# Kernel optimization log

Measured on AMD Instinct MI355X. Metric: run time of the kernel, lower is better.

Reference implementation:

```python
import jax, jax.numpy as jnp
import numpy as np

N_NODES = 100000
N_EDGES = 1600000
N_GRAPHS = 256
F_NODE, F_EDGE, HID, OUT = 64, 16, 128, 128
BN_SCALE = 1.0 / np.sqrt(1.0 + 1e-5)  # BatchNorm eval with running mean 0, var 1


def setup_inputs() -> dict:
    key = jax.random.key(0)
    ks = iter(jax.random.split(key, 64))
    inp = {}
    inp["x"] = jax.random.normal(next(ks), (N_NODES, F_NODE), dtype=jnp.float32)
    inp["edge_attr"] = jax.random.normal(next(ks), (N_EDGES, F_EDGE), dtype=jnp.float32)
    inp["edge_index"] = jax.random.randint(next(ks), (2, N_EDGES), 0, N_NODES)
    inp["batch"] = jnp.sort(jax.random.randint(next(ks), (N_NODES,), 0, N_GRAPHS))

    def p(shape, scale):
        return (jax.random.normal(next(ks), shape, dtype=jnp.float32) * scale)

    in_dims = [F_NODE, HID, HID]
    for i, d in enumerate(in_dims):
        inp[f"el_w{i}"] = p((F_EDGE, d), F_EDGE ** -0.5)
        inp[f"el_b{i}"] = jnp.zeros((d,), jnp.float32)
        inp[f"c{i}_w1"] = p((d, HID), d ** -0.5)
        inp[f"c{i}_b1"] = jnp.zeros((HID,), jnp.float32)
        inp[f"c{i}_g"] = jnp.ones((HID,), jnp.float32)
        inp[f"c{i}_bt"] = jnp.zeros((HID,), jnp.float32)
        inp[f"c{i}_w2"] = p((HID, HID), HID ** -0.5)
        inp[f"c{i}_b2"] = jnp.zeros((HID,), jnp.float32)
    inp["o_w1"] = p((HID, OUT), HID ** -0.5)
    inp["o_b1"] = jnp.zeros((OUT,), jnp.float32)
    inp["o_w2"] = p((OUT, OUT), OUT ** -0.5)
    inp["o_b2"] = jnp.zeros((OUT,), jnp.float32)
    return inp


def reference(x, edge_attr,
              el_w0, el_b0, c0_w1, c0_b1, c0_g, c0_bt, c0_w2, c0_b2,
              el_w1, el_b1, c1_w1, c1_b1, c1_g, c1_bt, c1_w2, c1_b2,
              el_w2, el_b2, c2_w1, c2_b1, c2_g, c2_bt, c2_w2, c2_b2,
              o_w1, o_b1, o_w2, o_b2,
              edge_index, batch):
    src, dst = edge_index[0], edge_index[1]
    n = x.shape[0]
    layers = [
        (el_w0, el_b0, c0_w1, c0_b1, c0_g, c0_bt, c0_w2, c0_b2),
        (el_w1, el_b1, c1_w1, c1_b1, c1_g, c1_bt, c1_w2, c1_b2),
        (el_w2, el_b2, c2_w1, c2_b1, c2_g, c2_bt, c2_w2, c2_b2),
    ]
    h = x
    for (ew, eb, w1, b1, g, bt, w2, b2) in layers:
        ea = edge_attr @ ew + eb                              # [E, d]
        msg = jax.nn.relu(h[src] + ea)                        # GINEConv message
        agg = jax.ops.segment_sum(msg, dst, num_segments=n)   # scatter-sum to targets
        hh = h + agg                                          # (1+eps)*x + aggr, eps=0
        hh = hh @ w1 + b1                                     # MLP: Linear
        hh = g * (hh * BN_SCALE) + bt                         # BatchNorm1d (eval)
        hh = jax.nn.relu(hh)
        hh = hh @ w2 + b2                                     # MLP: Linear
        h = jax.nn.relu(hh)                                   # dropout(p=0, eval) + act
    s = jax.ops.segment_sum(h, batch, num_segments=N_GRAPHS)
    cnt = jax.ops.segment_sum(jnp.ones((n,), h.dtype), batch, num_segments=N_GRAPHS)
    pooled = s / jnp.maximum(cnt, 1.0)[:, None]               # scatter-mean pooling
    out = jax.nn.relu(pooled @ o_w1 + o_b1) @ o_w2 + o_b2     # out_lin
    return out
```

## Files before the change

kernel.cpp:

```cpp
#include <hip/hip_runtime.h>
#include <hip/hip_fp16.h>
#include <cstdint>
#include <cstddef>

#define N_NODES_C  100000
#define N_EDGES_C  1600000
#define N_GRAPHS_C 256
#define HID_C      128
#define BN_SCALE_C 0.9999950000374997f

#define SCAN_B 1024
#define SCAN_NB ((N_NODES_C + SCAN_B - 1) / SCAN_B)

typedef _Float16 h2 __attribute__((ext_vector_type(2)));
typedef _Float16 h4 __attribute__((ext_vector_type(4)));
typedef _Float16 h8 __attribute__((ext_vector_type(8)));
typedef float    f4 __attribute__((ext_vector_type(4)));

struct __align__(16) EA8 { h2 p[4]; };
struct __align__(8)  HQ  { h2 a, b; };
struct __align__(16) H8 { __half2 v[4]; };

#if defined(__has_builtin)
#  if __has_builtin(__builtin_amdgcn_fdot2)
#    define HAVE_FDOT2 1
#  endif
#endif
#ifndef HAVE_FDOT2
#  define HAVE_FDOT2 0
#endif

__device__ __forceinline__ float fdot2_(h2 a, h2 b, float c)
{
#if HAVE_FDOT2
    return __builtin_amdgcn_fdot2(a, b, c, false);
#else
    return c + (float)a[0] * (float)b[0] + (float)a[1] * (float)b[1];
#endif
}

__global__ __launch_bounds__(256) void hist_kernel(
    const int* __restrict__ dst, int* __restrict__ counts, int n_edges)
{
    int e = blockIdx.x * 256 + threadIdx.x;
    if (e < n_edges) atomicAdd(&counts[dst[e]], 1);
}

__global__ __launch_bounds__(SCAN_B) void scan1_kernel(
    const int* __restrict__ counts, int* __restrict__ incl,
    int* __restrict__ blocksums, int n)
{
    __shared__ int sdata[SCAN_B];
    const int lid = threadIdx.x;
    const int i = blockIdx.x * SCAN_B + lid;
    sdata[lid] = (i < n) ? counts[i] : 0;
    __syncthreads();
#pragma unroll
    for (int off = 1; off < SCAN_B; off <<= 1) {
        int t = (lid >= off) ? sdata[lid - off] : 0;
        __syncthreads();
        sdata[lid] += t;
        __syncthreads();
    }
    if (i < n) incl[i] = sdata[lid];
    if (lid == SCAN_B - 1) blocksums[blockIdx.x] = sdata[lid];
}

__global__ void scan2_kernel(const int* __restrict__ blocksums,
                             int* __restrict__ blockoffs, int nb)
{
    if (threadIdx.x == 0 && blockIdx.x == 0) {
        int off = 0;
        for (int b = 0; b < nb; ++b) { blockoffs[b] = off; off += blocksums[b]; }
    }
}

__global__ __launch_bounds__(SCAN_B) void scan3_kernel(
    int* __restrict__ incl, const int* __restrict__ blockoffs, int n)
{
    const int i = blockIdx.x * SCAN_B + threadIdx.x;
    if (i < n) incl[i] += blockoffs[blockIdx.x];
}

__global__ __launch_bounds__(256) void initrows_kernel(
    const int* __restrict__ incl, const int* __restrict__ counts,
    int* __restrict__ rowstart, int* __restrict__ cursor, int n)
{
    const int i = blockIdx.x * 256 + threadIdx.x;
    if (i < n) {
        const int rs = incl[i] - counts[i];
        rowstart[i] = rs;
        cursor[i]   = rs;
    }
}

__global__ __launch_bounds__(256) void scatter_kernel(
    const int* __restrict__ src, const int* __restrict__ dst,
    int* __restrict__ cursor, int* __restrict__ perm_src,
    int* __restrict__ perm_eid, int n_edges)
{
    const int e = blockIdx.x * 256 + threadIdx.x;
    if (e < n_edges) {
        const int pos = atomicAdd(&cursor[dst[e]], 1);
        perm_src[pos] = src[e];
        perm_eid[pos] = e;
    }
}

__global__ __launch_bounds__(256) void permute_ea_f16_kernel(
    const float* __restrict__ edge_attr, const int* __restrict__ perm_eid,
    __half* __restrict__ ea_f16, int n_edges)
{
    const int j = blockIdx.x * 256 + threadIdx.x;
    if (j >= n_edges) return;
    const int eid = perm_eid[j];
    const float4* p = (const float4*)(edge_attr + (size_t)eid * 16);
    const float4 q0 = p[0], q1 = p[1], q2 = p[2], q3 = p[3];
    H8 a, b;
    a.v[0] = __floats2half2_rn(q0.x, q0.y);
    a.v[1] = __floats2half2_rn(q0.z, q0.w);
    a.v[2] = __floats2half2_rn(q1.x, q1.y);
    a.v[3] = __floats2half2_rn(q1.z, q1.w);
    b.v[0] = __floats2half2_rn(q2.x, q2.y);
    b.v[1] = __floats2half2_rn(q2.z, q2.w);
    b.v[2] = __floats2half2_rn(q3.x, q3.y);
    b.v[3] = __floats2half2_rn(q3.z, q3.w);
    H8* o = (H8*)(ea_f16 + (size_t)j * 16);
    o[0] = a;
    o[1] = b;
}

__global__ __launch_bounds__(256) void cast_f16_kernel(
    const float* __restrict__ in, _Float16* __restrict__ out, int n4)
{
    const int i = blockIdx.x * 256 + threadIdx.x;
    if (i >= n4) return;
    const float4 v = ((const float4*)in)[i];
    h4 o; o[0] = (_Float16)v.x; o[1] = (_Float16)v.y;
    o[2] = (_Float16)v.z; o[3] = (_Float16)v.w;
    *(h4*)(out + (size_t)i * 4) = o;
}

__global__ __launch_bounds__(256) void transpose_w_kernel(
    const float* __restrict__ w, _Float16* __restrict__ wt, int K, int N)
{
    const int i = blockIdx.x * 256 + threadIdx.x;
    if (i >= K * N) return;
    const int n = i / K;
    const int k = i - n * K;
    wt[(size_t)n * K + k] = (_Float16)w[(size_t)k * N + n];
}

template<int DIN, bool LASTL>
__global__ __launch_bounds__(128) void gine_layer_kernel(
    const _Float16* __restrict__ hin,
    const _Float16* __restrict__ ea16,
    const int* __restrict__ perm_src,
    const int* __restrict__ rowstart, const int* __restrict__ rowend,
    const float* __restrict__ ew, const float* __restrict__ eb,
    const _Float16* __restrict__ w1t, const float* __restrict__ b1,
    const float* __restrict__ gm, const float* __restrict__ bt,
    const _Float16* __restrict__ w2t, const float* __restrict__ b2,
    float* __restrict__ hout, _Float16* __restrict__ h16out, int n_tiles)
{
    constexpr int SXP = DIN + 8;
    constexpr int STP = HID_C + 8;
    __shared__ _Float16 s_x[2][16][SXP];
    __shared__ _Float16 s_t[2][16][STP];

    const int w    = threadIdx.x >> 6;
    const int lane = threadIdx.x & 63;
    int tile = blockIdx.x * 2 + w;
    if (tile >= n_tiles) tile = n_tiles - 1;
    const int node0 = tile * 16;

    constexpr int NQ  = DIN / 4;
    constexpr int GPW = 64 / NQ;
    constexpr int NPG = 16 / GPW;
    const int fq = lane & (NQ - 1);
    const int g  = lane / NQ;

    h2 ew2h[8][4];
#pragma unroll
    for (int k2 = 0; k2 < 8; ++k2)
#pragma unroll
        for (int fi = 0; fi < 4; ++fi) {
            h2 t;
            t[0] = (_Float16)ew[(size_t)(2 * k2)     * DIN + fq * 4 + fi];
            t[1] = (_Float16)ew[(size_t)(2 * k2 + 1) * DIN + fq * 4 + fi];
            ew2h[k2][fi] = t;
        }
    const float4 ebv = *(const float4*)(eb + fq * 4);

#pragma unroll
    for (int i = 0; i < NPG; ++i) {
        const int ni = g * NPG + i;
        const int v  = node0 + ni;
        const int s0 = rowstart[v];
        const int s1 = rowend[v];

        float4 acc = {0.f, 0.f, 0.f, 0.f};
        int j = s0;
        for (; j + 2 <= s1; j += 2) {
            const int sn0 = perm_src[j + 0];
            const int sn1 = perm_src[j + 1];
            const HQ hq0 = *(const HQ*)(hin + (size_t)sn0 * DIN + fq * 4);
            const HQ hq1 = *(const HQ*)(hin + (size_t)sn1 * DIN + fq * 4);
            const EA8* pe = (const EA8*)(ea16 + (size_t)j * 16);
            const EA8 a0 = pe[0], c0 = pe[1], a1 = pe[2], c1 = pe[3];
            float4 m0 = {ebv.x, ebv.y, ebv.z, ebv.w};
            float4 m1 = m0;
#pragma unroll
            for (int k = 0; k < 4; ++k) {
                m0.x = fdot2_(a0.p[k], ew2h[k][0], m0.x);
                m0.y = fdot2_(a0.p[k], ew2h[k][1], m0.y);
                m0.z = fdot2_(a0.p[k], ew2h[k][2], m0.z);
                m0.w = fdot2_(a0.p[k], ew2h[k][3], m0.w);
                m1.x = fdot2_(a1.p[k], ew2h[k][0], m1.x);
                m1.y = fdot2_(a1.p[k], ew2h[k][1], m1.y);
                m1.z = fdot2_(a1.p[k], ew2h[k][2], m1.z);
                m1.w = fdot2_(a1.p[k], ew2h[k][3], m1.w);
            }
#pragma unroll
            for (int k = 0; k < 4; ++k) {
                m0.x = fdot2_(c0.p[k], ew2h[4 + k][0], m0.x);
                m0.y = fdot2_(c0.p[k], ew2h[4 + k][1], m0.y);
                m0.z = fdot2_(c0.p[k], ew2h[4 + k][2], m0.z);
                m0.w = fdot2_(c0.p[k], ew2h[4 + k][3], m0.w);
                m1.x = fdot2_(c1.p[k], ew2h[4 + k][0], m1.x);
                m1.y = fdot2_(c1.p[k], ew2h[4 + k][1], m1.y);
                m1.z = fdot2_(c1.p[k], ew2h[4 + k][2], m1.z);
                m1.w = fdot2_(c1.p[k], ew2h[4 + k][3], m1.w);
            }
            acc.x += fmaxf(m0.x + (float)hq0.a[0], 0.f) + fmaxf(m1.x + (float)hq1.a[0], 0.f);
            acc.y += fmaxf(m0.y + (float)hq0.a[1], 0.f) + fmaxf(m1.y + (float)hq1.a[1], 0.f);
            acc.z += fmaxf(m0.z + (float)hq0.b[0], 0.f) + fmaxf(m1.z + (float)hq1.b[0], 0.f);
            acc.w += fmaxf(m0.w + (float)hq0.b[1], 0.f) + fmaxf(m1.w + (float)hq1.b[1], 0.f);
        }
        if (j < s1) {
            const int sn = perm_src[j];
            const HQ hq = *(const HQ*)(hin + (size_t)sn * DIN + fq * 4);
            const EA8* pe = (const EA8*)(ea16 + (size_t)j * 16);
            const EA8 a0 = pe[0], c0 = pe[1];
            float4 m0 = {ebv.x, ebv.y, ebv.z, ebv.w};
#pragma unroll
            for (int k = 0; k < 4; ++k) {
                m0.x = fdot2_(a0.p[k], ew2h[k][0], m0.x);
                m0.y = fdot2_(a0.p[k], ew2h[k][1], m0.y);
                m0.z = fdot2_(a0.p[k], ew2h[k][2], m0.z);
                m0.w = fdot2_(a0.p[k], ew2h[k][3], m0.w);
            }
#pragma unroll
            for (int k = 0; k < 4; ++k) {
                m0.x = fdot2_(c0.p[k], ew2h[4 + k][0], m0.x);
                m0.y = fdot2_(c0.p[k], ew2h[4 + k][1], m0.y);
                m0.z = fdot2_(c0.p[k], ew2h[4 + k][2], m0.z);
                m0.w = fdot2_(c0.p[k], ew2h[4 + k][3], m0.w);
            }
            acc.x += fmaxf(m0.x + (float)hq.a[0], 0.f);
            acc.y += fmaxf(m0.y + (float)hq.a[1], 0.f);
            acc.z += fmaxf(m0.z + (float)hq.b[0], 0.f);
            acc.w += fmaxf(m0.w + (float)hq.b[1], 0.f);
        }

        const HQ hv = *(const HQ*)(hin + (size_t)v * DIN + fq * 4);
        h4 o;
        o[0] = (_Float16)(acc.x + (float)hv.a[0]);
        o[1] = (_Float16)(acc.y + (float)hv.a[1]);
        o[2] = (_Float16)(acc.z + (float)hv.b[0]);
        o[3] = (_Float16)(acc.w + (float)hv.b[1]);
        *(h4*)&s_x[w][ni][fq * 4] = o;
    }
    __syncthreads();

    const int ln   = lane & 15;
    const int quad = lane >> 4;

#pragma unroll
    for (int nt = 0; nt < 8; ++nt) {
        const int col = nt * 16 + ln;
        const float bv = b1[col];
        f4 acc = {bv, bv, bv, bv};
#pragma unroll
        for (int ks = 0; ks < DIN / 32; ++ks) {
            const h8 af = *(const h8*)&s_x[w][ln][ks * 32 + quad * 8];
            const h8 bf = *(const h8*)(w1t + (size_t)col * DIN + ks * 32 + quad * 8);
            acc = __builtin_amdgcn_mfma_f32_16x16x32_f16(af, bf, acc, 0, 0, 0);
        }
        const float gv = gm[col], btv = bt[col];
#pragma unroll
        for (int r = 0; r < 4; ++r) {
            const float t = fmaxf(fmaf(acc[r] * BN_SCALE_C, gv, btv), 0.f);
            s_t[w][quad * 4 + r][col] = (_Float16)t;
        }
    }
    __syncthreads();

#pragma unroll
    for (int nt = 0; nt < 8; ++nt) {
        const int col = nt * 16 + ln;
        const float bv = b2[col];
        f4 acc = {bv, bv, bv, bv};
#pragma unroll
        for (int ks = 0; ks < HID_C / 32; ++ks) {
            const h8 af = *(const h8*)&s_t[w][ln][ks * 32 + quad * 8];
            const h8 bf = *(const h8*)(w2t + (size_t)col * HID_C + ks * 32 + quad * 8);
            acc = __builtin_amdgcn_mfma_f32_16x16x32_f16(af, bf, acc, 0, 0, 0);
        }
#pragma unroll
        for (int r = 0; r < 4; ++r) {
            const int node = node0 + quad * 4 + r;
            const float v = fmaxf(acc[r], 0.f);
            if (LASTL) {
                hout[(size_t)node * HID_C + col] = v;
            } else {
                h16out[(size_t)node * HID_C + col] = (_Float16)v;
            }
        }
    }
}

__global__ __launch_bounds__(256) void pool_kernel(
    const float* __restrict__ hfin, const int* __restrict__ batch,
    const float* __restrict__ w1, const float* __restrict__ b1,
    const float* __restrict__ w2, const float* __restrict__ b2,
    float* __restrict__ out, int n_nodes)
{
    const int gid = blockIdx.x;

    int lo = 0, hi = n_nodes;
    while (lo < hi) { int mid = (lo + hi) >> 1; if (batch[mid] < gid) lo = mid + 1; else hi = mid; }
    const int start = lo;
    hi = n_nodes;
    while (lo < hi) { int mid = (lo + hi) >> 1; if (batch[mid] < gid + 1) lo = mid + 1; else hi = mid; }
    const int end = lo;

    const int f = threadIdx.x & (HID_C - 1);
    const int half = threadIdx.x >> 7;

    float sum = 0.f;
    for (int n = start + half; n < end; n += 2)
        sum += hfin[(size_t)n * HID_C + f];

    __shared__ float s_sum[2][HID_C];
    __shared__ float s_p[HID_C];
    __shared__ float s_t[HID_C];
    s_sum[half][f] = sum;
    __syncthreads();

    if (threadIdx.x < HID_C) {
        const float cnt = (float)(end - start);
        s_p[f] = (s_sum[0][f] + s_sum[1][f]) / fmaxf(cnt, 1.f);
    }
    __syncthreads();

    if (threadIdx.x < HID_C) {
        float acc = b1[f];
        for (int k = 0; k < HID_C; ++k) acc = fmaf(s_p[k], w1[k * HID_C + f], acc);
        s_t[f] = fmaxf(acc, 0.f);
    }
    __syncthreads();

    if (threadIdx.x < HID_C) {
        float acc = b2[f];
        for (int k = 0; k < HID_C; ++k) acc = fmaf(s_t[k], w2[k * HID_C + f], acc);
        out[(size_t)gid * HID_C + f] = acc;
    }
}

extern "C" void kernel_launch(void* const* d_in, const int* in_sizes, int n_in,
                              void* d_out, int out_size, void* d_ws, size_t ws_size,
                              hipStream_t stream)
{
    const float* x         = (const float*)d_in[0];
    const float* edge_attr = (const float*)d_in[1];
    const int*   edge_index= (const int*)  d_in[2];
    const int*   batch     = (const int*)  d_in[3];
    const int*   src = edge_index;
    const int*   dst = edge_index + N_EDGES_C;

    const float* el_w[3] = {(const float*)d_in[4],  (const float*)d_in[12], (const float*)d_in[20]};
    const float* el_b[3] = {(const float*)d_in[5],  (const float*)d_in[13], (const float*)d_in[21]};
    const float* c_w1[3] = {(const float*)d_in[6],  (const float*)d_in[14], (const float*)d_in[22]};
    const float* c_b1[3] = {(const float*)d_in[7],  (const float*)d_in[15], (const float*)d_in[23]};
    const float* c_g [3] = {(const float*)d_in[8],  (const float*)d_in[16], (const float*)d_in[24]};
    const float* c_bt[3] = {(const float*)d_in[9],  (const float*)d_in[17], (const float*)d_in[25]};
    const float* c_w2[3] = {(const float*)d_in[10], (const float*)d_in[18], (const float*)d_in[26]};
    const float* c_b2[3] = {(const float*)d_in[11], (const float*)d_in[19], (const float*)d_in[27]};
    const float* o_w1 = (const float*)d_in[28];
    const float* o_b1 = (const float*)d_in[29];
    const float* o_w2 = (const float*)d_in[30];
    const float* o_b2 = (const float*)d_in[31];

    char* wsp = (char*)d_ws;
    size_t used = 0;
    auto alloc = [&](size_t bytes) { char* p = wsp + used; used += (bytes + 255) & ~(size_t)255; return p; };
    float* h        = (float*)alloc((size_t)N_NODES_C * HID_C * 4);
    int*   counts   = (int*)alloc((size_t)N_NODES_C * 4);
    int*   incl     = (int*)alloc((size_t)N_NODES_C * 4);
    int*   rowstart = (int*)alloc((size_t)N_NODES_C * 4);
    int*   cursor   = (int*)alloc((size_t)N_NODES_C * 4);
    int*   blocksums= (int*)alloc(128 * 4);
    int*   blockoffs= (int*)alloc(128 * 4);
    int*   perm_src = (int*)alloc((size_t)N_EDGES_C * 4);
    int*   perm_eid = (int*)alloc((size_t)N_EDGES_C * 4);
    _Float16* ea_f16 = (_Float16*)alloc((size_t)N_EDGES_C * 16 * 2);
    _Float16* h16_a  = (_Float16*)alloc((size_t)N_NODES_C * HID_C * 2);
    _Float16* h16_b  = (_Float16*)alloc((size_t)N_NODES_C * HID_C * 2);
    _Float16* x_f16  = (_Float16*)alloc((size_t)N_NODES_C * 64 * 2);
    _Float16* w1t[3], *w2t[3];
    for (int l = 0; l < 3; ++l) {
        w1t[l] = (_Float16*)alloc((size_t)HID_C * HID_C * 2);
        w2t[l] = (_Float16*)alloc((size_t)HID_C * HID_C * 2);
    }
    (void)ws_size;

    hipMemsetAsync(counts, 0, (size_t)N_NODES_C * 4, stream);
    hist_kernel<<<(N_EDGES_C + 255) / 256, 256, 0, stream>>>(dst, counts, N_EDGES_C);
    scan1_kernel<<<SCAN_NB, SCAN_B, 0, stream>>>(counts, incl, blocksums, N_NODES_C);
    scan2_kernel<<<1, 64, 0, stream>>>(blocksums, blockoffs, SCAN_NB);
    scan3_kernel<<<SCAN_NB, SCAN_B, 0, stream>>>(incl, blockoffs, N_NODES_C);
    initrows_kernel<<<(N_NODES_C + 255) / 256, 256, 0, stream>>>(incl, counts, rowstart,
                                                                 cursor, N_NODES_C);
    scatter_kernel<<<(N_EDGES_C + 255) / 256, 256, 0, stream>>>(src, dst, cursor,
                                                                perm_src, perm_eid, N_EDGES_C);
    permute_ea_f16_kernel<<<(N_EDGES_C + 255) / 256, 256, 0, stream>>>(
        edge_attr, perm_eid, (__half*)ea_f16, N_EDGES_C);
    cast_f16_kernel<<<(N_NODES_C * 64 / 4 + 255) / 256, 256, 0, stream>>>(
        x, x_f16, N_NODES_C * 64 / 4);
    for (int l = 0; l < 3; ++l) {
        const int K1 = (l == 0) ? 64 : HID_C;
        transpose_w_kernel<<<(K1 * HID_C + 255) / 256, 256, 0, stream>>>(
            c_w1[l], w1t[l], K1, HID_C);
        transpose_w_kernel<<<(HID_C * HID_C + 255) / 256, 256, 0, stream>>>(
            c_w2[l], w2t[l], HID_C, HID_C);
    }

    const int n_tiles = N_NODES_C / 16;
    const int nb = (n_tiles + 1) / 2;

    gine_layer_kernel<64, false><<<nb, 128, 0, stream>>>(
        x_f16, ea_f16, perm_src, rowstart, incl,
        el_w[0], el_b[0], w1t[0], c_b1[0], c_g[0], c_bt[0], w2t[0], c_b2[0],
        h, h16_a, n_tiles);
    gine_layer_kernel<128, false><<<nb, 128, 0, stream>>>(
        h16_a, ea_f16, perm_src, rowstart, incl,
        el_w[1], el_b[1], w1t[1], c_b1[1], c_g[1], c_bt[1], w2t[1], c_b2[1],
        h, h16_b, n_tiles);
    gine_layer_kernel<128, true><<<nb, 128, 0, stream>>>(
        h16_b, ea_f16, perm_src, rowstart, incl,
        el_w[2], el_b[2], w1t[2], c_b1[2], c_g[2], c_bt[2], w2t[2], c_b2[2],
        h, h16_a, n_tiles);

    pool_kernel<<<N_GRAPHS_C, 256, 0, stream>>>(h, batch, o_w1, o_b1, o_w2, o_b2,
                                                (float*)d_out, N_NODES_C);
}
```

Before: 1.048 ms.

## Split fused GINE layer into separate aggregation and MFMA MLP kernels

Each fused layer kernel is split in two. A gather/aggregation kernel assigns one node per thread group across 256-thread blocks and writes the aggregated fp16 features to a global buffer. A separate 64-thread MFMA kernel then runs the two-layer MLP per 16-node tile. The perm_src and perm_eid arrays are also merged into one interleaved int2 array. The aim is better load balance and occupancy in the irregular gather phase, with no node-tile imbalance stalling the MFMA stage, at the cost of an extra global round trip for the aggregated features and extra launches.

Measured after the change: 1.066 ms. No clear change (+1.8%).

```diff
diff --git a/kernel.cpp b/kernel.cpp
--- a/kernel.cpp
+++ b/kernel.cpp
@@ -19,7 +19,7 @@
 
 struct __align__(16) EA8 { h2 p[4]; };
 struct __align__(8)  HQ  { h2 a, b; };
-struct __align__(16) H8 { __half2 v[4]; };
+struct __align__(16) H8  { __half2 v[4]; };
 
 #if defined(__has_builtin)
 #  if __has_builtin(__builtin_amdgcn_fdot2)
@@ -96,24 +96,22 @@
 
 __global__ __launch_bounds__(256) void scatter_kernel(
     const int* __restrict__ src, const int* __restrict__ dst,
-    int* __restrict__ cursor, int* __restrict__ perm_src,
-    int* __restrict__ perm_eid, int n_edges)
+    int* __restrict__ cursor, int2* __restrict__ perm_se, int n_edges)
 {
     const int e = blockIdx.x * 256 + threadIdx.x;
     if (e < n_edges) {
         const int pos = atomicAdd(&cursor[dst[e]], 1);
-        perm_src[pos] = src[e];
-        perm_eid[pos] = e;
+        perm_se[pos] = make_int2(src[e], e);
     }
 }
 
 __global__ __launch_bounds__(256) void permute_ea_f16_kernel(
-    const float* __restrict__ edge_attr, const int* __restrict__ perm_eid,
+    const float* __restrict__ edge_attr, const int2* __restrict__ perm_se,
     __half* __restrict__ ea_f16, int n_edges)
 {
     const int j = blockIdx.x * 256 + threadIdx.x;
     if (j >= n_edges) return;
-    const int eid = perm_eid[j];
+    const int eid = perm_se[j].y;
     const float4* p = (const float4*)(edge_attr + (size_t)eid * 16);
     const float4 q0 = p[0], q1 = p[1], q2 = p[2], q3 = p[3];
     H8 a, b;
@@ -151,34 +149,20 @@
     wt[(size_t)n * K + k] = (_Float16)w[(size_t)k * N + n];
 }
 
-template<int DIN, bool LASTL>
-__global__ __launch_bounds__(128) void gine_layer_kernel(
-    const _Float16* __restrict__ hin,
-    const _Float16* __restrict__ ea16,
-    const int* __restrict__ perm_src,
+template<int DIN>
+__global__ __launch_bounds__(256) void gine_agg_kernel(
+    const _Float16* __restrict__ hin, const _Float16* __restrict__ ea16,
+    const int2* __restrict__ perm_se,
     const int* __restrict__ rowstart, const int* __restrict__ rowend,
     const float* __restrict__ ew, const float* __restrict__ eb,
-    const _Float16* __restrict__ w1t, const float* __restrict__ b1,
-    const float* __restrict__ gm, const float* __restrict__ bt,
-    const _Float16* __restrict__ w2t, const float* __restrict__ b2,
-    float* __restrict__ hout, _Float16* __restrict__ h16out, int n_tiles)
-{
-    constexpr int SXP = DIN + 8;
-    constexpr int STP = HID_C + 8;
-    __shared__ _Float16 s_x[2][16][SXP];
-    __shared__ _Float16 s_t[2][16][STP];
-
-    const int w    = threadIdx.x >> 6;
-    const int lane = threadIdx.x & 63;
-    int tile = blockIdx.x * 2 + w;
-    if (tile >= n_tiles) tile = n_tiles - 1;
-    const int node0 = tile * 16;
-
-    constexpr int NQ  = DIN / 4;
-    constexpr int GPW = 64 / NQ;
-    constexpr int NPG = 16 / GPW;
-    const int fq = lane & (NQ - 1);
-    const int g  = lane / NQ;
+    _Float16* __restrict__ x16, int n_nodes)
+{
+    constexpr int NQ    = DIN / 4;
+    constexpr int SLOTS = 256 / NQ;
+    const int fq   = threadIdx.x & (NQ - 1);
+    const int slot = threadIdx.x / NQ;
+    const int v = blockIdx.x * SLOTS + slot;
+    if (v >= n_nodes) return;
 
     h2 ew2h[8][4];
 #pragma unroll
@@ -192,89 +176,104 @@
         }
     const float4 ebv = *(const float4*)(eb + fq * 4);
 
-#pragma unroll
-    for (int i = 0; i < NPG; ++i) {
-        const int ni = g * NPG + i;
-        const int v  = node0 + ni;
-        const int s0 = rowstart[v];
-        const int s1 = rowend[v];
-
-        float4 acc = {0.f, 0.f, 0.f, 0.f};
-        int j = s0;
-        for (; j + 2 <= s1; j += 2) {
-            const int sn0 = perm_src[j + 0];
-            const int sn1 = perm_src[j + 1];
-            const HQ hq0 = *(const HQ*)(hin + (size_t)sn0 * DIN + fq * 4);
-            const HQ hq1 = *(const HQ*)(hin + (size_t)sn1 * DIN + fq * 4);
-            const EA8* pe = (const EA8*)(ea16 + (size_t)j * 16);
-            const EA8 a0 = pe[0], c0 = pe[1], a1 = pe[2], c1 = pe[3];
-            float4 m0 = {ebv.x, ebv.y, ebv.z, ebv.w};
-            float4 m1 = m0;
-#pragma unroll
-            for (int k = 0; k < 4; ++k) {
-                m0.x = fdot2_(a0.p[k], ew2h[k][0], m0.x);
-                m0.y = fdot2_(a0.p[k], ew2h[k][1], m0.y);
-                m0.z = fdot2_(a0.p[k], ew2h[k][2], m0.z);
-                m0.w = fdot2_(a0.p[k], ew2h[k][3], m0.w);
-                m1.x = fdot2_(a1.p[k], ew2h[k][0], m1.x);
-                m1.y = fdot2_(a1.p[k], ew2h[k][1], m1.y);
-                m1.z = fdot2_(a1.p[k], ew2h[k][2], m1.z);
-                m1.w = fdot2_(a1.p[k], ew2h[k][3], m1.w);
-            }
-#pragma unroll
-            for (int k = 0; k < 4; ++k) {
-                m0.x = fdot2_(c0.p[k], ew2h[4 + k][0], m0.x);
-                m0.y = fdot2_(c0.p[k], ew2h[4 + k][1], m0.y);
-                m0.z = fdot2_(c0.p[k], ew2h[4 + k][2], m0.z);
-                m0.w = fdot2_(c0.p[k], ew2h[4 + k][3], m0.w);
-                m1.x = fdot2_(c1.p[k], ew2h[4 + k][0], m1.x);
-                m1.y = fdot2_(c1.p[k], ew2h[4 + k][1], m1.y);
-                m1.z = fdot2_(c1.p[k], ew2h[4 + k][2], m1.z);
-                m1.w = fdot2_(c1.p[k], ew2h[4 + k][3], m1.w);
-            }
-            acc.x += fmaxf(m0.x + (float)hq0.a[0], 0.f) + fmaxf(m1.x + (float)hq1.a[0], 0.f);
-            acc.y += fmaxf(m0.y + (float)hq0.a[1], 0.f) + fmaxf(m1.y + (float)hq1.a[1], 0.f);
-            acc.z += fmaxf(m0.z + (float)hq0.b[0], 0.f) + fmaxf(m1.z + (float)hq1.b[0], 0.f);
-            acc.w += fmaxf(m0.w + (float)hq0.b[1], 0.f) + fmaxf(m1.w + (float)hq1.b[1], 0.f);
-        }
-        if (j < s1) {
-            const int sn = perm_src[j];
-            const HQ hq = *(const HQ*)(hin + (size_t)sn * DIN + fq * 4);
-            const EA8* pe = (const EA8*)(ea16 + (size_t)j * 16);
-            const EA8 a0 = pe[0], c0 = pe[1];
-            float4 m0 = {ebv.x, ebv.y, ebv.z, ebv.w};
-#pragma unroll
-            for (int k = 0; k < 4; ++k) {
-                m0.x = fdot2_(a0.p[k], ew2h[k][0], m0.x);
-                m0.y = fdot2_(a0.p[k], ew2h[k][1], m0.y);
-                m0.z = fdot2_(a0.p[k], ew2h[k][2], m0.z);
-                m0.w = fdot2_(a0.p[k], ew2h[k][3], m0.w);
-            }
-#pragma unroll
-            for (int k = 0; k < 4; ++k) {
-                m0.x = fdot2_(c0.p[k], ew2h[4 + k][0], m0.x);
-                m0.y = fdot2_(c0.p[k], ew2h[4 + k][1], m0.y);
-                m0.z = fdot2_(c0.p[k], ew2h[4 + k][2], m0.z);
-                m0.w = fdot2_(c0.p[k], ew2h[4 + k][3], m0.w);
-            }
-            acc.x += fmaxf(m0.x + (float)hq.a[0], 0.f);
-            acc.y += fmaxf(m0.y + (float)hq.a[1], 0.f);
-            acc.z += fmaxf(m0.z + (float)hq.b[0], 0.f);
-            acc.w += fmaxf(m0.w + (float)hq.b[1], 0.f);
-        }
-
-        const HQ hv = *(const HQ*)(hin + (size_t)v * DIN + fq * 4);
-        h4 o;
-        o[0] = (_Float16)(acc.x + (float)hv.a[0]);
-        o[1] = (_Float16)(acc.y + (float)hv.a[1]);
-        o[2] = (_Float16)(acc.z + (float)hv.b[0]);
-        o[3] = (_Float16)(acc.w + (float)hv.b[1]);
-        *(h4*)&s_x[w][ni][fq * 4] = o;
-    }
-    __syncthreads();
-
+    const int s0 = rowstart[v];
+    const int s1 = rowend[v];
+
+    float4 acc = {0.f, 0.f, 0.f, 0.f};
+    int j = s0;
+    for (; j + 2 <= s1; j += 2) {
+        const int sn0 = perm_se[j + 0].x;
+        const int sn1 = perm_se[j + 1].x;
+        const HQ hq0 = *(const HQ*)(hin + (size_t)sn0 * DIN + fq * 4);
+        const HQ hq1 = *(const HQ*)(hin + (size_t)sn1 * DIN + fq * 4);
+        const EA8* pe = (const EA8*)(ea16 + (size_t)j * 16);
+        const EA8 a0 = pe[0], c0 = pe[1], a1 = pe[2], c1 = pe[3];
+        float4 m0 = {ebv.x, ebv.y, ebv.z, ebv.w};
+        float4 m1 = m0;
+#pragma unroll
+        for (int k = 0; k < 4; ++k) {
+            m0.x = fdot2_(a0.p[k], ew2h[k][0], m0.x);
+            m0.y = fdot2_(a0.p[k], ew2h[k][1], m0.y);
+            m0.z = fdot2_(a0.p[k], ew2h[k][2], m0.z);
+            m0.w = fdot2_(a0.p[k], ew2h[k][3], m0.w);
+            m1.x = fdot2_(a1.p[k], ew2h[k][0], m1.x);
+            m1.y = fdot2_(a1.p[k], ew2h[k][1], m1.y);
+            m1.z = fdot2_(a1.p[k], ew2h[k][2], m1.z);
+            m1.w = fdot2_(a1.p[k], ew2h[k][3], m1.w);
+        }
+#pragma unroll
+        for (int k = 0; k < 4; ++k) {
+            m0.x = fdot2_(c0.p[k], ew2h[4 + k][0], m0.x);
+            m0.y = fdot2_(c0.p[k], ew2h[4 + k][1], m0.y);
+            m0.z = fdot2_(c0.p[k], ew2h[4 + k][2], m0.z);
+            m0.w = fdot2_(c0.p[k], ew2h[4 + k][3], m0.w);
+            m1.x = fdot2_(c1.p[k], ew2h[4 + k][0], m1.x);
+            m1.y = fdot2_(c1.p[k], ew2h[4 + k][1], m1.y);
+            m1.z = fdot2_(c1.p[k], ew2h[4 + k][2], m1.z);
+            m1.w = fdot2_(c1.p[k], ew2h[4 + k][3], m1.w);
+        }
+        acc.x += fmaxf(m0.x + (float)hq0.a[0], 0.f) + fmaxf(m1.x + (float)hq1.a[0], 0.f);
+        acc.y += fmaxf(m0.y + (float)hq0.a[1], 0.f) + fmaxf(m1.y + (float)hq1.a[1], 0.f);
+        acc.z += fmaxf(m0.z + (float)hq0.b[0], 0.f) + fmaxf(m1.z + (float)hq1.b[0], 0.f);
+        acc.w += fmaxf(m0.w + (float)hq0.b[1], 0.f) + fmaxf(m1.w + (float)hq1.b[1], 0.f);
+    }
+    if (j < s1) {
+        const int sn = perm_se[j].x;
+        const HQ hq = *(const HQ*)(hin + (size_t)sn * DIN + fq * 4);
+        const EA8* pe = (const EA8*)(ea16 + (size_t)j * 16);
+        const EA8 a0 = pe[0], c0 = pe[1];
+        float4 m0 = {ebv.x, ebv.y, ebv.z, ebv.w};
+#pragma unroll
+        for (int k = 0; k < 4; ++k) {
+            m0.x = fdot2_(a0.p[k], ew2h[k][0], m0.x);
+            m0.y = fdot2_(a0.p[k], ew2h[k][1], m0.y);
+            m0.z = fdot2_(a0.p[k], ew2h[k][2], m0.z);
+            m0.w = fdot2_(a0.p[k], ew2h[k][3], m0.w);
+        }
+#pragma unroll
+        for (int k = 0; k < 4; ++k) {
+            m0.x = fdot2_(c0.p[k], ew2h[4 + k][0], m0.x);
+            m0.y = fdot2_(c0.p[k], ew2h[4 + k][1], m0.y);
+            m0.z = fdot2_(c0.p[k], ew2h[4 + k][2], m0.z);
+            m0.w = fdot2_(c0.p[k], ew2h[4 + k][3], m0.w);
+        }
+        acc.x += fmaxf(m0.x + (float)hq.a[0], 0.f);
+        acc.y += fmaxf(m0.y + (float)hq.a[1], 0.f);
+        acc.z += fmaxf(m0.z + (float)hq.b[0], 0.f);
+        acc.w += fmaxf(m0.w + (float)hq.b[1], 0.f);
+    }
+
+    const HQ hv = *(const HQ*)(hin + (size_t)v * DIN + fq * 4);
+    h4 o;
+    o[0] = (_Float16)(acc.x + (float)hv.a[0]);
+    o[1] = (_Float16)(acc.y + (float)hv.a[1]);
+    o[2] = (_Float16)(acc.z + (float)hv.b[0]);
+    o[3] = (_Float16)(acc.w + (float)hv.b[1]);
+    *(h4*)(x16 + (size_t)v * DIN + fq * 4) = o;
+}
+
+template<int DIN, bool LASTL>
+__global__ __launch_bounds__(64) void node_mfma_kernel(
+    const _Float16* __restrict__ x16,
+    const _Float16* __restrict__ w1t, const float* __restrict__ b1,
+    const float* __restrict__ gm, const float* __restrict__ bt,
+    const _Float16* __restrict__ w2t, const float* __restrict__ b2,
+    float* __restrict__ hout, _Float16* __restrict__ h16out, int n_tiles)
+{
+    constexpr int STP = HID_C + 8;
+    __shared__ _Float16 s_t[16][STP];
+
+    const int lane = threadIdx.x;
+    const int tile = blockIdx.x;
+    const int node0 = tile * 16;
     const int ln   = lane & 15;
     const int quad = lane >> 4;
+
+    constexpr int NKS = DIN / 32;
+    h8 af[NKS];
+#pragma unroll
+    for (int ks = 0; ks < NKS; ++ks)
+        af[ks] = *(const h8*)(x16 + (size_t)(node0 + ln) * DIN + ks * 32 + quad * 8);
 
 #pragma unroll
     for (int nt = 0; nt < 8; ++nt) {
@@ -282,19 +281,23 @@
         const float bv = b1[col];
         f4 acc = {bv, bv, bv, bv};
 #pragma unroll
-        for (int ks = 0; ks < DIN / 32; ++ks) {
-            const h8 af = *(const h8*)&s_x[w][ln][ks * 32 + quad * 8];
+        for (int ks = 0; ks < NKS; ++ks) {
             const h8 bf = *(const h8*)(w1t + (size_t)col * DIN + ks * 32 + quad * 8);
-            acc = __builtin_amdgcn_mfma_f32_16x16x32_f16(af, bf, acc, 0, 0, 0);
+            acc = __builtin_amdgcn_mfma_f32_16x16x32_f16(af[ks], bf, acc, 0, 0, 0);
         }
         const float gv = gm[col], btv = bt[col];
 #pragma unroll
         for (int r = 0; r < 4; ++r) {
             const float t = fmaxf(fmaf(acc[r] * BN_SCALE_C, gv, btv), 0.f);
-            s_t[w][quad * 4 + r][col] = (_Float16)t;
+            s_t[quad * 4 + r][col] = (_Float16)t;
         }
     }
     __syncthreads();
+
+    h8 af2[4];
+#pragma unroll
+    for (int ks = 0; ks < 4; ++ks)
+        af2[ks] = *(const h8*)&s_t[ln][ks * 32 + quad * 8];
 
 #pragma unroll
     for (int nt = 0; nt < 8; ++nt) {
@@ -302,10 +305,9 @@
         const float bv = b2[col];
         f4 acc = {bv, bv, bv, bv};
 #pragma unroll
-        for (int ks = 0; ks < HID_C / 32; ++ks) {
-            const h8 af = *(const h8*)&s_t[w][ln][ks * 32 + quad * 8];
+        for (int ks = 0; ks < 4; ++ks) {
             const h8 bf = *(const h8*)(w2t + (size_t)col * HID_C + ks * 32 + quad * 8);
-            acc = __builtin_amdgcn_mfma_f32_16x16x32_f16(af, bf, acc, 0, 0, 0);
+            acc = __builtin_amdgcn_mfma_f32_16x16x32_f16(af2[ks], bf, acc, 0, 0, 0);
         }
 #pragma unroll
         for (int r = 0; r < 4; ++r) {
@@ -402,9 +404,9 @@
     int*   cursor   = (int*)alloc((size_t)N_NODES_C * 4);
     int*   blocksums= (int*)alloc(128 * 4);
     int*   blockoffs= (int*)alloc(128 * 4);
-    int*   perm_src = (int*)alloc((size_t)N_EDGES_C * 4);
-    int*   perm_eid = (int*)alloc((size_t)N_EDGES_C * 4);
+    int2*  perm_se  = (int2*)alloc((size_t)N_EDGES_C * 8);
     _Float16* ea_f16 = (_Float16*)alloc((size_t)N_EDGES_C * 16 * 2);
+    _Float16* x16    = (_Float16*)alloc((size_t)N_NODES_C * HID_C * 2);
     _Float16* h16_a  = (_Float16*)alloc((size_t)N_NODES_C * HID_C * 2);
     _Float16* h16_b  = (_Float16*)alloc((size_t)N_NODES_C * HID_C * 2);
     _Float16* x_f16  = (_Float16*)alloc((size_t)N_NODES_C * 64 * 2);
@@ -423,9 +425,9 @@
     initrows_kernel<<<(N_NODES_C + 255) / 256, 256, 0, stream>>>(incl, counts, rowstart,
                                                                  cursor, N_NODES_C);
     scatter_kernel<<<(N_EDGES_C + 255) / 256, 256, 0, stream>>>(src, dst, cursor,
-                                                                perm_src, perm_eid, N_EDGES_C);
+                                                                perm_se, N_EDGES_C);
     permute_ea_f16_kernel<<<(N_EDGES_C + 255) / 256, 256, 0, stream>>>(
-        edge_attr, perm_eid, (__half*)ea_f16, N_EDGES_C);
+        edge_attr, perm_se, (__half*)ea_f16, N_EDGES_C);
     cast_f16_kernel<<<(N_NODES_C * 64 / 4 + 255) / 256, 256, 0, stream>>>(
         x, x_f16, N_NODES_C * 64 / 4);
     for (int l = 0; l < 3; ++l) {
@@ -437,19 +439,24 @@
     }
 
     const int n_tiles = N_NODES_C / 16;
-    const int nb = (n_tiles + 1) / 2;
-
-    gine_layer_kernel<64, false><<<nb, 128, 0, stream>>>(
-        x_f16, ea_f16, perm_src, rowstart, incl,
-        el_w[0], el_b[0], w1t[0], c_b1[0], c_g[0], c_bt[0], w2t[0], c_b2[0],
+
+    gine_agg_kernel<64><<<(N_NODES_C + 15) / 16, 256, 0, stream>>>(
+        x_f16, ea_f16, perm_se, rowstart, incl, el_w[0], el_b[0],
+        x16, N_NODES_C);
+    node_mfma_kernel<64, false><<<n_tiles, 64, 0, stream>>>(
+        x16, w1t[0], c_b1[0], c_g[0], c_bt[0], w2t[0], c_b2[0],
         h, h16_a, n_tiles);
-    gine_layer_kernel<128, false><<<nb, 128, 0, stream>>>(
-        h16_a, ea_f16, perm_src, rowstart, incl,
-        el_w[1], el_b[1], w1t[1], c_b1[1], c_g[1], c_bt[1], w2t[1], c_b2[1],
+    gine_agg_kernel<128><<<(N_NODES_C + 7) / 8, 256, 0, stream>>>(
+        h16_a, ea_f16, perm_se, rowstart, incl, el_w[1], el_b[1],
+        x16, N_NODES_C);
+    node_mfma_kernel<128, false><<<n_tiles, 64, 0, stream>>>(
+        x16, w1t[1], c_b1[1], c_g[1], c_bt[1], w2t[1], c_b2[1],
         h, h16_b, n_tiles);
-    gine_layer_kernel<128, true><<<nb, 128, 0, stream>>>(
-        h16_b, ea_f16, perm_src, rowstart, incl,
-        el_w[2], el_b[2], w1t[2], c_b1[2], c_g[2], c_bt[2], w2t[2], c_b2[2],
+    gine_agg_kernel<128><<<(N_NODES_C + 7) / 8, 256, 0, stream>>>(
+        h16_b, ea_f16, perm_se, rowstart, incl, el_w[2], el_b[2],
+        x16, N_NODES_C);
+    node_mfma_kernel<128, true><<<n_tiles, 64, 0, stream>>>(
+        x16, w1t[2], c_b1[2], c_g[2], c_bt[2], w2t[2], c_b2[2],
         h, h16_a, n_tiles);
 
     pool_kernel<<<N_GRAPHS_C, 256, 0, stream>>>(h, batch, o_w1, o_b1, o_w2, o_b2,
```
